# Performance work log

Measured on AMD Instinct MI355X. Metric: run time of the kernel, lower is better.

## Reference

```python
import jax, jax.numpy as jnp
import numpy as np

KH, KW = 3, 3
STRIDE = 1
OUT_C = 512


def im2col(x, kh, kw, stride):
    # x: [N, C, H, W] -> col: [C*kh*kw, N*oh*ow]  (row order: C major, then kh, kw)
    N, C, H, W = x.shape
    oh = (H - kh) // stride + 1
    ow = (W - kw) // stride + 1
    rows = jnp.arange(oh)[:, None] * stride + jnp.arange(kh)[None, :]  # [oh, kh]
    cols = jnp.arange(ow)[:, None] * stride + jnp.arange(kw)[None, :]  # [ow, kw]
    # gather windows: result [N, C, oh, kh, ow, kw]
    A = x[:, :, rows[:, :, None, None], cols[None, None, :, :]]
    # permute to (C, kh, kw, N, oh, ow) then flatten, matching torch permute(1,4,5,0,2,3)
    col = jnp.transpose(A, (1, 3, 5, 0, 2, 4)).reshape(C * kh * kw, N * oh * ow)
    return col, oh, ow


def setup_inputs() -> dict:
    key = jax.random.key(0)
    k1, k2, k3 = jax.random.split(key, 3)
    N, C, H, W = 16, 256, 32, 32
    K_sel = (C * KH * KW) // 2  # 1152 rows kept by the binary mask
    x = jax.random.normal(k1, (N, C, H, W), dtype=jnp.float32)
    weight = jax.random.normal(k2, (K_sel, OUT_C), dtype=jnp.float32) * 0.02
    idx = jnp.sort(jax.random.randint(k3, (K_sel,), 0, C * KH * KW, dtype=jnp.int32))
    return {"x": x, "weight": weight, "idx": idx}


def reference(x, weight, idx):
    N = x.shape[0]
    col, oh, ow = im2col(x, KH, KW, STRIDE)          # [C*kh*kw, N*oh*ow]
    x_tile = col[idx, :].T                            # gather masked rows -> [N*oh*ow, K_sel]
    conv_out = x_tile @ weight                        # [N*oh*ow, out_c]
    conv_out = conv_out.reshape(N, oh * ow, OUT_C)
    conv_out = jnp.transpose(conv_out, (0, 2, 1)).reshape(N, OUT_C, oh, ow)
    return conv_out
```

## Files before the change

kernel.cpp:

```cpp
#include <hip/hip_runtime.h>
#include <stdint.h>

#define N_IMG   16
#define C_IN    256
#define H_IN    32
#define W_IN    32
#define OH      30
#define OW      30
#define K_SEL   1152
#define OUTC    512
#define RY_TOT  (N_IMG * OH)
#define M_HAT   (RY_TOT * 32)
#define X_ELEMS (N_IMG * C_IN * H_IN * W_IN)
#define OUT_SP  (OH * OW)
#define CHW     (C_IN * H_IN * W_IN)

#define TO      128
#define TM      64
#define NMT     (M_HAT / TM)
#define NOT     (OUTC / TO)
#define BSTR    40
#define KITER   (K_SEL / 32)

#define NPACK   (NMT * KITER)
#define NPREPW  (36 * 16)
#define WTF_BYTES 1179648u
#define BF_BYTES  35389440u

typedef float f32x4  __attribute__((ext_vector_type(4)));
typedef short bf16x8 __attribute__((ext_vector_type(8)));

__device__ __forceinline__ unsigned short f2bf(float f) {
    unsigned int u = __float_as_uint(f);
    u += 0x7FFFu + ((u >> 16) & 1u);
    return (unsigned short)(u >> 16);
}

__device__ __forceinline__ void gl_lds16(const void* g, void* lds) {
    __builtin_amdgcn_global_load_lds(
        (const __attribute__((address_space(1))) unsigned int*)g,
        (__attribute__((address_space(3))) unsigned int*)lds,
        16, 0, 0);
}


__global__ void prepA_kernel(const int* __restrict__ idx, const float* __restrict__ w,
                             const float* __restrict__ x,
                             unsigned short* __restrict__ wTf,
                             unsigned short* __restrict__ Bf) {
    __shared__ float tile[32][33];
    const int bid = blockIdx.x, t = threadIdx.x;

    if (bid < NPACK) {
        const int mt = bid / KITER, kt = bid - mt * KITER;
        const int lane = t & 63, ns = t >> 6;
        const int quad = lane >> 4, lo = lane & 15;
        const int m  = ns * 16 + lo;
        const int ry = m >> 5, xw = m & 31;
        const int ryg = mt * 2 + ry;
        const int n = ryg / 30, y = ryg - n * 30;
        const int base = n * CHW + y * W_IN + min(xw, 29);
        unsigned int uu[4];
#pragma unroll
        for (int jp = 0; jp < 4; ++jp) {
            unsigned short ua, ub;
            {
                int k = kt * 32 + quad * 8 + jp * 2;
                int v = idx[k];
                int c = v / 9, rem = v - c * 9;
                int i = rem / 3, j2 = rem - i * 3;
                ua = f2bf(x[base + c * (H_IN * W_IN) + i * W_IN + j2]);
            }
            {
                int k = kt * 32 + quad * 8 + jp * 2 + 1;
                int v = idx[k];
                int c = v / 9, rem = v - c * 9;
                int i = rem / 3, j2 = rem - i * 3;
                ub = f2bf(x[base + c * (H_IN * W_IN) + i * W_IN + j2]);
            }
            uu[jp] = (unsigned int)ua | ((unsigned int)ub << 16);
        }
        uint4 pk; pk.x = uu[0]; pk.y = uu[1]; pk.z = uu[2]; pk.w = uu[3];
        *reinterpret_cast<uint4*>(&Bf[(size_t)bid * 2048 + t * 8]) = pk;
    } else {
        const int b = bid - NPACK;
        const int bx = b % 36, by = b / 36;
        const int s0 = bx * 32, o0 = by * 32;
        const int oc = t & 31, sg = t >> 5;
#pragma unroll
        for (int i = 0; i < 4; ++i) {
            int sl = sg * 4 + i;
            tile[sl][oc] = w[(s0 + sl) * OUTC + o0 + oc];
        }
        __syncthreads();
        const int ol = t >> 3, sq = t & 7;
        unsigned int u0 = (unsigned int)f2bf(tile[sq * 4 + 0][ol]) |
                          ((unsigned int)f2bf(tile[sq * 4 + 1][ol]) << 16);
        unsigned int u1 = (unsigned int)f2bf(tile[sq * 4 + 2][ol]) |
                          ((unsigned int)f2bf(tile[sq * 4 + 3][ol]) << 16);
        uint2 pk; pk.x = u0; pk.y = u1;
        const size_t fi =
            (((((size_t)(by >> 1) * KITER + bx) * 4 + ((by * 2 + (ol >> 4)) & 3)) * 64
              + (sq >> 1) * 16 + (ol & 15)) * 8) + (sq & 1) * 4;
        *reinterpret_cast<uint2*>(&wTf[fi]) = pk;
    }
}

__global__ __launch_bounds__(256, 4)
void gemmA_kernel(const unsigned short* __restrict__ wTf,
                  const unsigned short* __restrict__ Bf,
                  float* __restrict__ out) {
    __shared__ __align__(16) unsigned short Bs[2][2048];

    const int t    = threadIdx.x;
    const int wave = t >> 6;
    const int lane = t & 63;
    const int quad = lane >> 4;
    const int lo   = lane & 15;

    const int bid = blockIdx.x;
    const int mt  = bid % NMT;
    const int ot  = bid / NMT;
    const int oBase = ot * TO;
    const int mBase = mt * TM;

    const int ow64 = ot * 2 + (wave >> 1);
    const int idx0 = (wave * 2) & 3;
    const unsigned short* aP =
        wTf + ((size_t)ow64 * KITER * 4 + idx0) * 512 + (size_t)lane * 8;
    const unsigned short* bfP =
        Bf + (size_t)mt * KITER * 2048 + wave * 512 + (size_t)lane * 8;

    unsigned short* ldst0 = &Bs[0][wave * 512];
    unsigned short* ldst1 = &Bs[1][wave * 512];
    const unsigned short* bRd0 = &Bs[0][lane * 8];
    const unsigned short* bRd1 = &Bs[1][lane * 8];

    f32x4 acc[2][4] = {};
    bf16x8 aR[2][2];

    gl_lds16(bfP, ldst0);
    aR[0][0] = *(const bf16x8*)(aP);
    aR[0][1] = *(const bf16x8*)(aP + 512);
    asm volatile("s_waitcnt vmcnt(2)" ::: "memory");
    __builtin_amdgcn_s_barrier();

#pragma unroll 2
    for (int kt = 0; kt < KITER; ++kt) {
        const int p = kt & 1, q = p ^ 1;
        const int k1 = (kt + 1 < KITER ? kt + 1 : KITER - 1);

        gl_lds16(bfP + (size_t)k1 * 2048, q ? ldst1 : ldst0);
        aR[q][0] = *(const bf16x8*)(aP + (size_t)(k1 * 4) * 512);
        aR[q][1] = *(const bf16x8*)(aP + (size_t)(k1 * 4 + 1) * 512);

        bf16x8 b[4];
        const unsigned short* br = p ? bRd1 : bRd0;
#pragma unroll
        for (int ns = 0; ns < 4; ++ns)
            b[ns] = *(const bf16x8*)(br + ns * 512);
        asm volatile("s_waitcnt lgkmcnt(0)" ::: "memory");
        __builtin_amdgcn_sched_barrier(0);
        asm volatile("s_waitcnt vmcnt(3)" ::: "memory");

#pragma unroll
        for (int ms = 0; ms < 2; ++ms)
#pragma unroll
            for (int ns = 0; ns < 4; ++ns)
                acc[ms][ns] = __builtin_amdgcn_mfma_f32_16x16x32_bf16(
                    aR[p][ms], b[ns], acc[ms][ns], 0, 0, 0);

        asm volatile("s_waitcnt vmcnt(2)" ::: "memory");
        __builtin_amdgcn_s_barrier();
    }

#pragma unroll
    for (int ns = 0; ns < 4; ++ns) {
        const int mh  = mBase + ns * 16 + lo;
        const int xwe = mh & 31;
        const int ryg = mh >> 5;
        const int n = ryg / 30, y = ryg - n * 30;
        if (xwe < OW) {
            const size_t ob = (size_t)n * (OUTC * OUT_SP) + (size_t)y * OW + xwe;
#pragma unroll
            for (int ms = 0; ms < 2; ++ms) {
                const int o0 = oBase + wave * 32 + ms * 16 + quad * 4;
#pragma unroll
                for (int r = 0; r < 4; ++r)
                    out[ob + (size_t)(o0 + r) * OUT_SP] = acc[ms][ns][r];
            }
        }
    }
}

__global__ void prepB_kernel(const int* __restrict__ idx, const float* __restrict__ w,
                             int* __restrict__ koff, unsigned short* __restrict__ wTf) {
    __shared__ float tile[32][33];
    const int bx = blockIdx.x, by = blockIdx.y, t = threadIdx.x;
    if (by == 0) {
        int k = bx * 256 + t;
        if (k < K_SEL) {
            int v = idx[k];
            int c = v / 9, rem = v - c * 9;
            int i = rem / 3, j = rem - i * 3;
            koff[k] = c * (H_IN * W_IN) + i * W_IN + j;
        }
    }
    const int s0 = bx * 32, o0 = by * 32;
    const int oc = t & 31, sg = t >> 5;
#pragma unroll
    for (int i = 0; i < 4; ++i) {
        int sl = sg * 4 + i;
        tile[sl][oc] = w[(s0 + sl) * OUTC + o0 + oc];
    }
    __syncthreads();
    const int ol = t >> 3, sq = t & 7;
    unsigned int u0 = (unsigned int)f2bf(tile[sq * 4 + 0][ol]) |
                      ((unsigned int)f2bf(tile[sq * 4 + 1][ol]) << 16);
    unsigned int u1 = (unsigned int)f2bf(tile[sq * 4 + 2][ol]) |
                      ((unsigned int)f2bf(tile[sq * 4 + 3][ol]) << 16);
    uint2 pk; pk.x = u0; pk.y = u1;
    const size_t fi =
        (((((size_t)(by >> 1) * KITER + bx) * 4 + ((by * 2 + (ol >> 4)) & 3)) * 64
          + (sq >> 1) * 16 + (ol & 15)) * 8) + (sq & 1) * 4;
    *reinterpret_cast<uint2*>(&wTf[fi]) = pk;
}

__global__ __launch_bounds__(256, 4)
void gemmB_kernel(const unsigned short* __restrict__ wTf, const float* __restrict__ x,
                  const int* __restrict__ koff, float* __restrict__ out) {
    __shared__ __align__(16) unsigned short Bs[2][TM * BSTR];
    __shared__ int koS[K_SEL];
    const int t = threadIdx.x, wave = t >> 6, lane = t & 63;
    const int quad = lane >> 4, lo = lane & 15;
    const int bid = blockIdx.x, mt = bid % NMT, ot = bid / NMT;
    const int oBase = ot * TO, mBase = mt * TM;
    for (int i = t; i < K_SEL; i += 256) koS[i] = koff[i];
    const int xw = t & 31, xwc = min(xw, 29);
    int basex[2];
#pragma unroll
    for (int ry = 0; ry < 2; ++ry) {
        int ryg = mt * 2 + ry;
        int n = ryg / 30, y = ryg - n * 30;
        basex[ry] = n * CHW + y * W_IN + xwc;
    }
    const int kq4 = t >> 5, ks = kq4 * 4;
    const int ow64 = ot * 2 + (wave >> 1);
    const int idx0 = (wave * 2) & 3;
    const unsigned short* aP =
        wTf + ((size_t)ow64 * KITER * 4 + idx0) * 512 + (size_t)lane * 8;
    const unsigned short* bB[2] = {
        &Bs[0][lo * BSTR + quad * 8], &Bs[1][lo * BSTR + quad * 8] };
    unsigned short* bW[2] = {
        &Bs[0][xw * BSTR + ks], &Bs[1][xw * BSTR + ks] };
    __syncthreads();
    f32x4 acc[2][4] = {};
    bf16x8 aR[2][2];
    float v[2][2][4];
    {
        int4 k4 = *(const int4*)&koS[ks];
#pragma unroll
        for (int ry = 0; ry < 2; ++ry)
#pragma unroll
            for (int j = 0; j < 4; ++j)
                v[0][ry][j] = x[basex[ry] + ((const int*)&k4)[j]];
    }
    asm volatile("s_waitcnt vmcnt(0)" ::: "memory");
#pragma unroll
    for (int ry = 0; ry < 2; ++ry) {
        unsigned int u0 = (unsigned int)f2bf(v[0][ry][0]) |
                          ((unsigned int)f2bf(v[0][ry][1]) << 16);
        unsigned int u1 = (unsigned int)f2bf(v[0][ry][2]) |
                          ((unsigned int)f2bf(v[0][ry][3]) << 16);
        uint2 pk; pk.x = u0; pk.y = u1;
        *reinterpret_cast<uint2*>(bW[0] + ry * 32 * BSTR) = pk;
    }
#pragma unroll
    for (int ms = 0; ms < 2; ++ms)
        aR[0][ms] = *(const bf16x8*)(aP + (size_t)ms * 512);
    {
        int4 k4 = *(const int4*)&koS[32 + ks];
#pragma unroll
        for (int ry = 0; ry < 2; ++ry)
#pragma unroll
            for (int j = 0; j < 4; ++j)
                v[1][ry][j] = x[basex[ry] + ((const int*)&k4)[j]];
    }
    asm volatile("s_waitcnt lgkmcnt(0)" ::: "memory");
    __builtin_amdgcn_s_barrier();
#pragma unroll 2
    for (int kt = 0; kt < KITER; ++kt) {
        const int p = kt & 1, q = p ^ 1;
        bf16x8 b[4];
#pragma unroll
        for (int ns = 0; ns < 4; ++ns)
            b[ns] = *(const bf16x8*)(bB[p] + ns * 16 * BSTR);
        {
            const int k1 = (kt + 1 < KITER ? kt + 1 : KITER - 1);
#pragma unroll
            for (int ms = 0; ms < 2; ++ms)
                aR[q][ms] = *(const bf16x8*)(aP + (size_t)(k1 * 4 + ms) * 512);
        }
        {
            const int k2 = (kt + 2 < KITER ? kt + 2 : KITER - 1) * 32;
            int4 k4 = *(const int4*)&koS[k2 + ks];
#pragma unroll
            for (int ry = 0; ry < 2; ++ry)
#pragma unroll
                for (int j = 0; j < 4; ++j)
                    v[p][ry][j] = x[basex[ry] + ((const int*)&k4)[j]];
        }
        asm volatile("s_waitcnt vmcnt(10)" ::: "memory");
        asm volatile("s_waitcnt lgkmcnt(0)" ::: "memory");
        __builtin_amdgcn_sched_barrier(0);
#pragma unroll
        for (int ry = 0; ry < 2; ++ry) {
            unsigned int u0 = (unsigned int)f2bf(v[q][ry][0]) |
                              ((unsigned int)f2bf(v[q][ry][1]) << 16);
            unsigned int u1 = (unsigned int)f2bf(v[q][ry][2]) |
                              ((unsigned int)f2bf(v[q][ry][3]) << 16);
            uint2 pk; pk.x = u0; pk.y = u1;
            *reinterpret_cast<uint2*>(bW[q] + ry * 32 * BSTR) = pk;
        }
#pragma unroll
        for (int ms = 0; ms < 2; ++ms)
#pragma unroll
            for (int ns = 0; ns < 4; ++ns)
                acc[ms][ns] = __builtin_amdgcn_mfma_f32_16x16x32_bf16(
                    aR[p][ms], b[ns], acc[ms][ns], 0, 0, 0);
        asm volatile("s_waitcnt lgkmcnt(0)" ::: "memory");
        __builtin_amdgcn_s_barrier();
    }
#pragma unroll
    for (int ns = 0; ns < 4; ++ns) {
        const int mh  = mBase + ns * 16 + lo;
        const int xwe = mh & 31;
        const int ryg = mh >> 5;
        const int n = ryg / 30, y = ryg - n * 30;
        if (xwe < OW) {
            const size_t ob = (size_t)n * (OUTC * OUT_SP) + (size_t)y * OW + xwe;
#pragma unroll
            for (int ms = 0; ms < 2; ++ms) {
                const int o0 = oBase + wave * 32 + ms * 16 + quad * 4;
#pragma unroll
                for (int r = 0; r < 4; ++r)
                    out[ob + (size_t)(o0 + r) * OUT_SP] = acc[ms][ns][r];
            }
        }
    }
}

extern "C" void kernel_launch(void* const* d_in, const int* in_sizes, int n_in,
                              void* d_out, int out_size, void* d_ws, size_t ws_size,
                              hipStream_t stream) {
    const float* x   = (const float*)d_in[0];
    const float* w   = (const float*)d_in[1];
    const int*   idx = (const int*)d_in[2];
    float*       out = (float*)d_out;
    char* ws = (char*)d_ws;

    if (ws_size >= (size_t)WTF_BYTES + BF_BYTES) {
        unsigned short* wTf = (unsigned short*)ws;
        unsigned short* Bf  = (unsigned short*)(ws + WTF_BYTES);
        prepA_kernel<<<dim3(NPACK + NPREPW), dim3(256), 0, stream>>>(
            idx, w, x, wTf, Bf);
        gemmA_kernel<<<dim3(NMT * NOT), dim3(256), 0, stream>>>(wTf, Bf, out);
    } else {
        int*            koff = (int*)ws;
        unsigned short* wTf  = (unsigned short*)(ws + 4608);
        prepB_kernel<<<dim3(K_SEL / 32, OUTC / 32), dim3(256), 0, stream>>>(
            idx, w, koff, wTf);
        gemmB_kernel<<<dim3(NMT * NOT), dim3(256), 0, stream>>>(wTf, x, koff, out);
    }
}
```

Measured before the change: 103.7 us.

## Deepen GEMM B-tile LDS pipeline to four stages and cache idx decode

The GEMM kernel grows its B-tile LDS ring from two to four buffers and prefetches two k-steps ahead. The per-iteration vmcnt wait before the barrier is dropped, which relies on the earlier vmcnt(3) to guarantee the tile is ready. The goal is to hide global-to-LDS latency better, at the cost of twice the LDS per block, which could limit occupancy. Separately, the packing kernel decodes the 32 idx entries per block once into shared memory, instead of every thread redoing the index load and div/mod math.

After: 102.6 us. About the same (-1.1%).

```diff
diff --git a/kernel.cpp b/kernel.cpp
--- a/kernel.cpp
+++ b/kernel.cpp
@@ -49,10 +49,18 @@
                              unsigned short* __restrict__ wTf,
                              unsigned short* __restrict__ Bf) {
     __shared__ float tile[32][33];
+    __shared__ int koS2[32];
     const int bid = blockIdx.x, t = threadIdx.x;
 
     if (bid < NPACK) {
         const int mt = bid / KITER, kt = bid - mt * KITER;
+        if (t < 32) {
+            int v = idx[kt * 32 + t];
+            int c = v / 9, rem = v - c * 9;
+            int i = rem / 3, j = rem - i * 3;
+            koS2[t] = c * (H_IN * W_IN) + i * W_IN + j;
+        }
+        __syncthreads();
         const int lane = t & 63, ns = t >> 6;
         const int quad = lane >> 4, lo = lane & 15;
         const int m  = ns * 16 + lo;
@@ -63,21 +71,9 @@
         unsigned int uu[4];
 #pragma unroll
         for (int jp = 0; jp < 4; ++jp) {
-            unsigned short ua, ub;
-            {
-                int k = kt * 32 + quad * 8 + jp * 2;
-                int v = idx[k];
-                int c = v / 9, rem = v - c * 9;
-                int i = rem / 3, j2 = rem - i * 3;
-                ua = f2bf(x[base + c * (H_IN * W_IN) + i * W_IN + j2]);
-            }
-            {
-                int k = kt * 32 + quad * 8 + jp * 2 + 1;
-                int v = idx[k];
-                int c = v / 9, rem = v - c * 9;
-                int i = rem / 3, j2 = rem - i * 3;
-                ub = f2bf(x[base + c * (H_IN * W_IN) + i * W_IN + j2]);
-            }
+            const int k0 = quad * 8 + jp * 2;
+            unsigned short ua = f2bf(x[base + koS2[k0]]);
+            unsigned short ub = f2bf(x[base + koS2[k0 + 1]]);
             uu[jp] = (unsigned int)ua | ((unsigned int)ub << 16);
         }
         uint4 pk; pk.x = uu[0]; pk.y = uu[1]; pk.z = uu[2]; pk.w = uu[3];
@@ -110,7 +106,7 @@
 void gemmA_kernel(const unsigned short* __restrict__ wTf,
                   const unsigned short* __restrict__ Bf,
                   float* __restrict__ out) {
-    __shared__ __align__(16) unsigned short Bs[2][2048];
+    __shared__ __align__(16) unsigned short Bs[4][2048];
 
     const int t    = threadIdx.x;
     const int wave = t >> 6;
@@ -131,34 +127,38 @@
     const unsigned short* bfP =
         Bf + (size_t)mt * KITER * 2048 + wave * 512 + (size_t)lane * 8;
 
-    unsigned short* ldst0 = &Bs[0][wave * 512];
-    unsigned short* ldst1 = &Bs[1][wave * 512];
-    const unsigned short* bRd0 = &Bs[0][lane * 8];
-    const unsigned short* bRd1 = &Bs[1][lane * 8];
+    unsigned short* ldst[4] = {
+        &Bs[0][wave * 512], &Bs[1][wave * 512],
+        &Bs[2][wave * 512], &Bs[3][wave * 512] };
+    const unsigned short* bRd[4] = {
+        &Bs[0][lane * 8], &Bs[1][lane * 8],
+        &Bs[2][lane * 8], &Bs[3][lane * 8] };
 
     f32x4 acc[2][4] = {};
     bf16x8 aR[2][2];
 
-    gl_lds16(bfP, ldst0);
+    gl_lds16(bfP, ldst[0]);
+    gl_lds16(bfP + 2048, ldst[1]);
     aR[0][0] = *(const bf16x8*)(aP);
     aR[0][1] = *(const bf16x8*)(aP + 512);
     asm volatile("s_waitcnt vmcnt(2)" ::: "memory");
     __builtin_amdgcn_s_barrier();
 
-#pragma unroll 2
+#pragma unroll 4
     for (int kt = 0; kt < KITER; ++kt) {
         const int p = kt & 1, q = p ^ 1;
+        const int c = kt & 3;
         const int k1 = (kt + 1 < KITER ? kt + 1 : KITER - 1);
-
-        gl_lds16(bfP + (size_t)k1 * 2048, q ? ldst1 : ldst0);
+        const int k2 = (kt + 2 < KITER ? kt + 2 : KITER - 1);
+
+        gl_lds16(bfP + (size_t)k2 * 2048, ldst[(kt + 2) & 3]);
         aR[q][0] = *(const bf16x8*)(aP + (size_t)(k1 * 4) * 512);
         aR[q][1] = *(const bf16x8*)(aP + (size_t)(k1 * 4 + 1) * 512);
 
         bf16x8 b[4];
-        const unsigned short* br = p ? bRd1 : bRd0;
 #pragma unroll
         for (int ns = 0; ns < 4; ++ns)
-            b[ns] = *(const bf16x8*)(br + ns * 512);
+            b[ns] = *(const bf16x8*)(bRd[c] + ns * 512);
         asm volatile("s_waitcnt lgkmcnt(0)" ::: "memory");
         __builtin_amdgcn_sched_barrier(0);
         asm volatile("s_waitcnt vmcnt(3)" ::: "memory");
@@ -170,7 +170,6 @@
                 acc[ms][ns] = __builtin_amdgcn_mfma_f32_16x16x32_bf16(
                     aR[p][ms], b[ns], acc[ms][ns], 0, 0, 0);
 
-        asm volatile("s_waitcnt vmcnt(2)" ::: "memory");
         __builtin_amdgcn_s_barrier();
     }
 
```
